# Optimization experiments

Hardware: AMD Instinct MI355X
Metric: run time of the kernel (lower is better)

Reference implementation:

```python
import jax, jax.numpy as jnp
import numpy as np

K = 7          # kernel_size
PAD = 3        # padding
EPS = 1e-8


def setup_inputs() -> dict:
    key = jax.random.key(0)
    x = jax.random.normal(key, (32, 3, 512, 512), dtype=jnp.float32)
    return {"x": x}


def reference(x) -> jnp.ndarray:
    # Faithful fused version of: unfold -> center/neighbor cosine distance -> sum/8.
    # stride=1, dilation=1, padding=3, kernel=7 => output spatial size == input size,
    # and the patch center (flat index 24) is exactly the unpadded pixel itself.
    B, C, H, W = x.shape
    xp = jnp.pad(x, ((0, 0), (0, 0), (PAD, PAD), (PAD, PAD)))
    center = x  # == xp[:, :, PAD:PAD+H, PAD:PAD+W]
    # ||center|| over channels, clamped (matches .norm(dim=1).clamp_min(eps))
    cn = jnp.maximum(jnp.sqrt(jnp.sum(center * center, axis=1)), EPS)  # (B,H,W)
    acc = jnp.zeros((B, H, W), dtype=x.dtype)
    mid = K // 2
    for i in range(K):  # small fixed 7x7 loop; avoids materializing (B,C,49,H*W)
        for j in range(K):
            if i == mid and j == mid:
                continue  # skip center (neighbor_idx excludes center_flat)
            nb = xp[:, :, i:i + H, j:j + W]                      # (B,C,H,W)
            dot = jnp.sum(center * nb, axis=1)                   # (B,H,W)
            nn_ = jnp.maximum(jnp.sqrt(jnp.sum(nb * nb, axis=1)), EPS)
            acc = acc + (1.0 - dot / (cn * nn_))
    out = acc / 8.0  # module hardcodes /8 despite 48 neighbors
    return out[:, None, :, :]  # (B,1,H,W)
```

## Files before the change

kernel.cpp:

```cpp
#include <hip/hip_runtime.h>


typedef unsigned int u32;
typedef float f32x2 __attribute__((ext_vector_type(2)));
typedef float f32x4 __attribute__((ext_vector_type(4)));

#define EPS2 1e-16f

constexpr int HR = 14;

__device__ __forceinline__ u32 packbf2(float a, float b) {
    const u32 ua = __float_as_uint(a) + 0x8000u;
    const u32 ub = __float_as_uint(b) + 0x8000u;
    return __builtin_amdgcn_perm(ub, ua, 0x07060302u);
}
__device__ __forceinline__ float uplo(u32 u) { return __uint_as_float(u << 16); }
__device__ __forceinline__ float uphi(u32 u) { return __uint_as_float(u & 0xffff0000u); }
__device__ __forceinline__ f32x2 up2(u32 u) {
    f32x2 r; r.x = uplo(u); r.y = uphi(u); return r;
}
__device__ __forceinline__ f32x4 vmul(f32x4 v, float s) {
    f32x4 r; r[0]=v[0]*s; r[1]=v[1]*s; r[2]=v[2]*s; r[3]=v[3]*s; return r;
}

__global__ __launch_bounds__(256, 4) void mcnd_kernel(const float* __restrict__ x,
                                                      float* __restrict__ out,
                                                      int B, int H, int W) {
    __shared__ uint4 hsh[4][3][HR][8];

    const int HW = H * W;
    const int tilesX = W >> 6;
    const int tilesPerImg = tilesX * (H >> 5);

    const int cpx  = gridDim.x >> 3;
    const int wgid = (blockIdx.x & 7) * cpx + (blockIdx.x >> 3);
    const int b    = wgid / tilesPerImg;
    const int t    = wgid % tilesPerImg;
    const int ty   = t / tilesX;
    const int tx   = t - ty * tilesX;
    const int x0   = tx << 6;

    const int wv   = threadIdx.x >> 6;
    const int lane = threadIdx.x & 63;
    const int r    = lane >> 3;
    const int grp  = lane & 7;
    const int yw   = (ty << 5) + (wv << 3);

    const float* __restrict__ xb = x + (size_t)b * 3 * HW;

    const int   gxl   = x0 + (grp << 3) - 4;
    const float lmask = (gxl >= 0) ? 1.f : 0.f;
    const float rmask = (gxl + 16 <= W) ? 1.f : 0.f;
    const int   gofL  = (gxl >= 0) ? gxl : 0;
    const int   gofR  = (gxl + 16 <= W) ? (gxl + 12) : (W - 4);

    u32 gc0[4], gc1[4], gc2[4];

    auto process = [&](int hr, bool capture) {
        const int   gy  = yw + hr - 3;
        const float rmk = (gy >= 0 && gy < H) ? 1.f : 0.f;
        const int   gyc = gy < 0 ? 0 : (gy >= H ? H - 1 : gy);
        const float* rp0 = xb + (size_t)gyc * W;
        const float* rp1 = rp0 + HW;
        const float* rp2 = rp1 + HW;
        f32x4 a0 = *(const f32x4*)(rp0 + gofL);
        f32x4 a1 = *(const f32x4*)(rp0 + gxl + 4);
        f32x4 a2 = *(const f32x4*)(rp0 + gxl + 8);
        f32x4 a3 = *(const f32x4*)(rp0 + gofR);
        f32x4 b0 = *(const f32x4*)(rp1 + gofL);
        f32x4 b1 = *(const f32x4*)(rp1 + gxl + 4);
        f32x4 b2 = *(const f32x4*)(rp1 + gxl + 8);
        f32x4 b3 = *(const f32x4*)(rp1 + gofR);
        f32x4 c0 = *(const f32x4*)(rp2 + gofL);
        f32x4 c1 = *(const f32x4*)(rp2 + gxl + 4);
        f32x4 c2 = *(const f32x4*)(rp2 + gxl + 8);
        f32x4 c3 = *(const f32x4*)(rp2 + gofR);
        a0 = vmul(a0, lmask); b0 = vmul(b0, lmask); c0 = vmul(c0, lmask);
        a3 = vmul(a3, rmask); b3 = vmul(b3, rmask); c3 = vmul(c3, rmask);
        f32x4 i0, i1, i2, i3;
        {
            const f32x4 n0 = a0*a0 + b0*b0 + c0*c0;
            const f32x4 n1 = a1*a1 + b1*b1 + c1*c1;
            const f32x4 n2 = a2*a2 + b2*b2 + c2*c2;
            const f32x4 n3 = a3*a3 + b3*b3 + c3*c3;
#pragma unroll
            for (int e = 0; e < 4; ++e) {
                i0[e] = __builtin_amdgcn_rsqf(fmaxf(n0[e], EPS2)) * rmk;
                i1[e] = __builtin_amdgcn_rsqf(fmaxf(n1[e], EPS2)) * rmk;
                i2[e] = __builtin_amdgcn_rsqf(fmaxf(n2[e], EPS2)) * rmk;
                i3[e] = __builtin_amdgcn_rsqf(fmaxf(n3[e], EPS2)) * rmk;
            }
        }
        auto chan = [&](const f32x4& A0, const f32x4& A1, const f32x4& A2,
                        const f32x4& A3, int ch, u32* gcp) {
            float cc[16];
#pragma unroll
            for (int e = 0; e < 4; ++e) {
                cc[e]      = A0[e] * i0[e];
                cc[4 + e]  = A1[e] * i1[e];
                cc[8 + e]  = A2[e] * i2[e];
                cc[12 + e] = A3[e] * i3[e];
            }
            float hp[8];
            hp[0] = cc[1]+cc[2]+cc[3]+cc[4]+cc[5]+cc[6]+cc[7];
#pragma unroll
            for (int m = 1; m < 8; ++m) hp[m] = hp[m-1] - cc[m] + cc[m+7];
            uint4 hwv;
            hwv.x = packbf2(hp[0], hp[1]); hwv.y = packbf2(hp[2], hp[3]);
            hwv.z = packbf2(hp[4], hp[5]); hwv.w = packbf2(hp[6], hp[7]);
            hsh[wv][ch][hr][grp] = hwv;
            if (capture) {
                gcp[0] = packbf2(cc[4],  cc[5]);
                gcp[1] = packbf2(cc[6],  cc[7]);
                gcp[2] = packbf2(cc[8],  cc[9]);
                gcp[3] = packbf2(cc[10], cc[11]);
            }
        };
        chan(a0, a1, a2, a3, 0, gc0);
        chan(b0, b1, b2, b3, 1, gc1);
        chan(c0, c1, c2, c3, 2, gc2);
    };

    process(r + 3, true);
    if (lane < 48) {
        const int rr = lane >> 3;
        process(rr < 3 ? rr : rr + 8, false);
    }
    asm volatile("s_waitcnt lgkmcnt(0)" ::: "memory");
    __builtin_amdgcn_sched_barrier(0);

    f32x2 D[4];
#pragma unroll
    for (int e = 0; e < 4; ++e) D[e] = f32x2{0.f, 0.f};
    auto vch = [&](int ch, const u32* gcp) {
        f32x2 s[4];
#pragma unroll
        for (int e = 0; e < 4; ++e) s[e] = f32x2{0.f, 0.f};
#pragma unroll
        for (int d = 0; d < 7; ++d) {
            const uint4 u = hsh[wv][ch][r + d][grp];
            s[0] += up2(u.x);
            s[1] += up2(u.y);
            s[2] += up2(u.z);
            s[3] += up2(u.w);
        }
#pragma unroll
        for (int e = 0; e < 4; ++e) {
            D[e] += up2(gcp[e]) * s[e];
        }
    };
    vch(0, gc0); vch(1, gc1); vch(2, gc2);

    f32x4 o0, o1;
#pragma unroll
    for (int e = 0; e < 4; ++e) {
        const f32x2 v = (f32x2{49.f, 49.f} - D[e]) * 0.125f;
        if (e < 2) { o0[2*e] = v.x; o0[2*e + 1] = v.y; }
        else       { o1[2*(e-2)] = v.x; o1[2*(e-2) + 1] = v.y; }
    }
    float* op = out + (size_t)b * HW + (size_t)(yw + r) * W + (x0 + (grp << 3));
    *(f32x4*)(op)     = o0;
    *(f32x4*)(op + 4) = o1;
}

extern "C" void kernel_launch(void* const* d_in, const int* in_sizes, int n_in,
                              void* d_out, int out_size, void* d_ws, size_t ws_size,
                              hipStream_t stream) {
    (void)n_in; (void)d_ws; (void)ws_size; (void)out_size;
    const float* x = (const float*)d_in[0];
    float* out = (float*)d_out;

    const int H = 512, W = 512, C = 3;
    const int B = in_sizes[0] / (C * H * W);

    const int tilesPerImg = (W >> 6) * (H >> 5);
    mcnd_kernel<<<B * tilesPerImg, 256, 0, stream>>>(x, out, B, H, W);
}
```

Measured before the change: 35.32 us.

## Stream 32 rows per wave through a shared-memory ring buffer to cut halo reloads

Each wave now covers 32 output rows instead of 8. It walks down in four 8-row steps, keeping horizontal partial sums in a 16-slot LDS ring buffer and recovering the needed center values from the previous step through lane shuffles. This removes most of the 6-row vertical halo recomputation and reloads per tile, cutting redundant global loads and rsq work. The cost is a 4x smaller grid (fewer blocks for latency hiding), serial dependence across steps, and extra shuffles. The tile index math is now hardcoded for 512x512.

```diff
diff --git a/kernel.cpp b/kernel.cpp
--- a/kernel.cpp
+++ b/kernel.cpp
@@ -6,8 +6,6 @@
 typedef float f32x4 __attribute__((ext_vector_type(4)));
 
 #define EPS2 1e-16f
-
-constexpr int HR = 14;
 
 __device__ __forceinline__ u32 packbf2(float a, float b) {
     const u32 ua = __float_as_uint(a) + 0x8000u;
@@ -26,25 +24,23 @@
 __global__ __launch_bounds__(256, 4) void mcnd_kernel(const float* __restrict__ x,
                                                       float* __restrict__ out,
                                                       int B, int H, int W) {
-    __shared__ uint4 hsh[4][3][HR][8];
+    __shared__ uint4 hring[4][3][16][8];
 
     const int HW = H * W;
-    const int tilesX = W >> 6;
-    const int tilesPerImg = tilesX * (H >> 5);
 
     const int cpx  = gridDim.x >> 3;
     const int wgid = (blockIdx.x & 7) * cpx + (blockIdx.x >> 3);
-    const int b    = wgid / tilesPerImg;
-    const int t    = wgid % tilesPerImg;
-    const int ty   = t / tilesX;
-    const int tx   = t - ty * tilesX;
+    const int b    = wgid >> 5;
+    const int t    = wgid & 31;
+    const int tb   = t >> 3;
+    const int tx   = t & 7;
     const int x0   = tx << 6;
 
     const int wv   = threadIdx.x >> 6;
     const int lane = threadIdx.x & 63;
     const int r    = lane >> 3;
     const int grp  = lane & 7;
-    const int yw   = (ty << 5) + (wv << 3);
+    const int yw   = (tb << 7) + (wv << 5);
 
     const float* __restrict__ xb = x + (size_t)b * 3 * HW;
 
@@ -54,10 +50,8 @@
     const int   gofL  = (gxl >= 0) ? gxl : 0;
     const int   gofR  = (gxl + 16 <= W) ? (gxl + 12) : (W - 4);
 
-    u32 gc0[4], gc1[4], gc2[4];
-
-    auto process = [&](int hr, bool capture) {
-        const int   gy  = yw + hr - 3;
+    auto process = [&](int n, u32* gcp) {
+        const int   gy  = yw + n;
         const float rmk = (gy >= 0 && gy < H) ? 1.f : 0.f;
         const int   gyc = gy < 0 ? 0 : (gy >= H ? H - 1 : gy);
         const float* rp0 = xb + (size_t)gyc * W;
@@ -91,8 +85,9 @@
                 i3[e] = __builtin_amdgcn_rsqf(fmaxf(n3[e], EPS2)) * rmk;
             }
         }
+        const int slot = n & 15;
         auto chan = [&](const f32x4& A0, const f32x4& A1, const f32x4& A2,
-                        const f32x4& A3, int ch, u32* gcp) {
+                        const f32x4& A3, int ch) {
             float cc[16];
 #pragma unroll
             for (int e = 0; e < 4; ++e) {
@@ -108,59 +103,91 @@
             uint4 hwv;
             hwv.x = packbf2(hp[0], hp[1]); hwv.y = packbf2(hp[2], hp[3]);
             hwv.z = packbf2(hp[4], hp[5]); hwv.w = packbf2(hp[6], hp[7]);
-            hsh[wv][ch][hr][grp] = hwv;
-            if (capture) {
-                gcp[0] = packbf2(cc[4],  cc[5]);
-                gcp[1] = packbf2(cc[6],  cc[7]);
-                gcp[2] = packbf2(cc[8],  cc[9]);
-                gcp[3] = packbf2(cc[10], cc[11]);
+            hring[wv][ch][slot][grp] = hwv;
+            if (gcp) {
+                gcp[ch*4 + 0] = packbf2(cc[4],  cc[5]);
+                gcp[ch*4 + 1] = packbf2(cc[6],  cc[7]);
+                gcp[ch*4 + 2] = packbf2(cc[8],  cc[9]);
+                gcp[ch*4 + 3] = packbf2(cc[10], cc[11]);
             }
         };
-        chan(a0, a1, a2, a3, 0, gc0);
-        chan(b0, b1, b2, b3, 1, gc1);
-        chan(c0, c1, c2, c3, 2, gc2);
+        chan(a0, a1, a2, a3, 0);
+        chan(b0, b1, b2, b3, 1);
+        chan(c0, c1, c2, c3, 2);
     };
 
-    process(r + 3, true);
-    if (lane < 48) {
-        const int rr = lane >> 3;
-        process(rr < 3 ? rr : rr + 8, false);
+    auto vertical = [&](int s, const u32* ctr) {
+        const int n0 = 8*s + r - 3;
+        f32x2 D[4];
+#pragma unroll
+        for (int e = 0; e < 4; ++e) D[e] = f32x2{0.f, 0.f};
+#pragma unroll
+        for (int ch = 0; ch < 3; ++ch) {
+            f32x2 sum[4];
+#pragma unroll
+            for (int e = 0; e < 4; ++e) sum[e] = f32x2{0.f, 0.f};
+#pragma unroll
+            for (int d = 0; d < 7; ++d) {
+                const uint4 u = hring[wv][ch][(n0 + d) & 15][grp];
+                sum[0] += up2(u.x); sum[1] += up2(u.y);
+                sum[2] += up2(u.z); sum[3] += up2(u.w);
+            }
+#pragma unroll
+            for (int e = 0; e < 4; ++e) D[e] += up2(ctr[ch*4 + e]) * sum[e];
+        }
+        f32x4 o0, o1;
+#pragma unroll
+        for (int e = 0; e < 4; ++e) {
+            const f32x2 v = (f32x2{49.f, 49.f} - D[e]) * 0.125f;
+            if (e < 2) { o0[2*e] = v.x; o0[2*e+1] = v.y; }
+            else       { o1[2*(e-2)] = v.x; o1[2*(e-2)+1] = v.y; }
+        }
+        float* op = out + (size_t)b * HW + (size_t)(yw + 8*s + r) * W
+                        + (x0 + (grp << 3));
+        *(f32x4*)(op)     = o0;
+        *(f32x4*)(op + 4) = o1;
+    };
+
+    u32 cur[12], prv[12];
+
+    {
+        u32 gB[12];
+#pragma unroll
+        for (int i = 0; i < 12; ++i) gB[i] = 0;
+        process(3 + r, cur);
+        if (lane < 48) process((lane >> 3) - 3, gB);
+        asm volatile("s_waitcnt lgkmcnt(0)" ::: "memory");
+        __builtin_amdgcn_sched_barrier(0);
+        u32 ctr[12];
+        const int iA = (lane >= 24) ? lane - 24 : 0;
+        const int iB = (lane < 24) ? lane + 24 : 47;
+#pragma unroll
+        for (int i = 0; i < 12; ++i) {
+            const u32 tA = (u32)__shfl((int)cur[i], iA);
+            const u32 tB = (u32)__shfl((int)gB[i],  iB);
+            ctr[i] = (r < 3) ? tB : tA;
+        }
+        vertical(0, ctr);
+#pragma unroll
+        for (int i = 0; i < 12; ++i) prv[i] = cur[i];
     }
-    asm volatile("s_waitcnt lgkmcnt(0)" ::: "memory");
-    __builtin_amdgcn_sched_barrier(0);
-
-    f32x2 D[4];
-#pragma unroll
-    for (int e = 0; e < 4; ++e) D[e] = f32x2{0.f, 0.f};
-    auto vch = [&](int ch, const u32* gcp) {
-        f32x2 s[4];
-#pragma unroll
-        for (int e = 0; e < 4; ++e) s[e] = f32x2{0.f, 0.f};
-#pragma unroll
-        for (int d = 0; d < 7; ++d) {
-            const uint4 u = hsh[wv][ch][r + d][grp];
-            s[0] += up2(u.x);
-            s[1] += up2(u.y);
-            s[2] += up2(u.z);
-            s[3] += up2(u.w);
-        }
-#pragma unroll
-        for (int e = 0; e < 4; ++e) {
-            D[e] += up2(gcp[e]) * s[e];
-        }
-    };
-    vch(0, gc0); vch(1, gc1); vch(2, gc2);
-
-    f32x4 o0, o1;
-#pragma unroll
-    for (int e = 0; e < 4; ++e) {
-        const f32x2 v = (f32x2{49.f, 49.f} - D[e]) * 0.125f;
-        if (e < 2) { o0[2*e] = v.x; o0[2*e + 1] = v.y; }
-        else       { o1[2*(e-2)] = v.x; o1[2*(e-2) + 1] = v.y; }
+
+#pragma unroll
+    for (int s = 1; s < 4; ++s) {
+        process(8*s + 3 + r, cur);
+        asm volatile("s_waitcnt lgkmcnt(0)" ::: "memory");
+        __builtin_amdgcn_sched_barrier(0);
+        u32 ctr[12];
+        const int idx = (r < 3) ? lane + 40 : lane - 24;
+#pragma unroll
+        for (int i = 0; i < 12; ++i) {
+            const u32 mix = (lane >= 40) ? prv[i] : cur[i];
+            ctr[i] = (u32)__shfl((int)mix, idx);
+        }
+        vertical(s, ctr);
+#pragma unroll
+        for (int i = 0; i < 12; ++i) prv[i] = cur[i];
     }
-    float* op = out + (size_t)b * HW + (size_t)(yw + r) * W + (x0 + (grp << 3));
-    *(f32x4*)(op)     = o0;
-    *(f32x4*)(op + 4) = o1;
 }
 
 extern "C" void kernel_launch(void* const* d_in, const int* in_sizes, int n_in,
@@ -173,6 +200,6 @@
     const int H = 512, W = 512, C = 3;
     const int B = in_sizes[0] / (C * H * W);
 
-    const int tilesPerImg = (W >> 6) * (H >> 5);
-    mcnd_kernel<<<B * tilesPerImg, 256, 0, stream>>>(x, out, B, H, W);
-}
+    const int blocks = B * (W >> 6) * (H >> 7);
+    mcnd_kernel<<<blocks, 256, 0, stream>>>(x, out, B, H, W);
+}
```

After: 39.90 us. +13.0%, slower.
